# Kernel optimization log

Hardware: AMD Instinct MI355X
Metric: run time of the kernel (lower is better)

The kernel has to match this reference:

```python
import jax, jax.numpy as jnp
import numpy as np

UNITS = 1024
B, T, D1, D2 = 16, 2048, 1024, 1024


def setup_inputs() -> dict:
    key = jax.random.key(0)
    ks = jax.random.split(key, 9)
    s1 = 1.0 / np.sqrt(D1)
    s2 = 1.0 / np.sqrt(D2)
    sw = 1.0 / np.sqrt(2 * UNITS)
    return {
        "sequences1": jax.random.normal(ks[0], (B, T, D1), dtype=jnp.float32),
        "sequences2": jax.random.normal(ks[1], (B, T, D2), dtype=jnp.float32),
        "W1_kernel": jax.random.normal(ks[2], (D1, UNITS), dtype=jnp.float32) * s1,
        "W1_bias": jnp.zeros((UNITS,), dtype=jnp.float32),
        "W2_kernel": jax.random.normal(ks[3], (D2, UNITS), dtype=jnp.float32) * s2,
        "W2_bias": jnp.zeros((UNITS,), dtype=jnp.float32),
        "W_kernel": jax.random.normal(ks[4], (2 * UNITS, UNITS), dtype=jnp.float32) * sw,
        "W_bias": jnp.zeros((UNITS,), dtype=jnp.float32),
        "context_vector": jax.random.uniform(ks[5], (UNITS, 1), dtype=jnp.float32),
    }


def reference(sequences1, sequences2, W1_kernel, W1_bias, W2_kernel, W2_bias,
              W_kernel, W_bias, context_vector):
    # Dense projections: [B,T,D] @ [D,U] -> [B,T,U]
    features1 = jnp.einsum("btd,du->btu", sequences1, W1_kernel) + W1_bias
    features2 = jnp.einsum("btd,du->btu", sequences2, W2_kernel) + W2_bias
    fusion = jnp.concatenate([features1, features2], axis=-1)  # [B,T,2U]
    features = jnp.tanh(jnp.einsum("btk,ku->btu", fusion, W_kernel) + W_bias)  # [B,T,U]
    # scores: [B,T,U] @ [U,1] -> [B,T,1]; softmax over time (axis=1)
    scores = jnp.einsum("btu,uo->bto", features, context_vector)
    attn = jax.nn.softmax(scores, axis=1)  # [B,T,1]
    # weighted sum over time: [B,T] x [B,T,U] -> [B,U]
    seq_rep = jnp.einsum("bt,btu->bu", attn[..., 0], features)
    return seq_rep
```

## Files before the change

kernel.cpp:

```cpp
#include <hip/hip_runtime.h>
#include <hip/hip_bf16.h>
#include <cstdint>
#include <cstddef>


typedef __attribute__((ext_vector_type(8))) short short8;
typedef __attribute__((ext_vector_type(4))) float f32x4;
typedef __attribute__((ext_vector_type(4))) unsigned short u16x4;

#define DEVINL static __device__ __forceinline__

DEVINL unsigned short bf16_rne(float f) {
  uint32_t u = __float_as_uint(f);
  uint32_t r = (u + 0x7FFFu + ((u >> 16) & 1u)) >> 16;
  return (unsigned short)r;
}
DEVINL float bf16f(unsigned short h) { return __uint_as_float(((uint32_t)h) << 16); }

DEVINL int lds_chunk(int r, int q) { return (r << 2) + (q ^ ((r >> 1) & 3)); }

DEVINL void gload_lds16(const void* g, void* l) {
  __builtin_amdgcn_global_load_lds(
      (const __attribute__((address_space(1))) uint32_t*)g,
      (__attribute__((address_space(3))) uint32_t*)l, 16, 0, 0);
}

DEVINL float fast_tanh(float x) {
  float e = __expf(2.0f * x);
  return 1.0f - 2.0f / (e + 1.0f);
}

template<int MFR, int NFR, int WMW, int WNW, int MODE>
__global__ __launch_bounds__(WMW*WNW*64, 2)
void gemm3x(const float* __restrict__ A1, const float* __restrict__ A2,
            const unsigned short* __restrict__ Bh, const unsigned short* __restrict__ Bl,
            unsigned short* __restrict__ Mh, unsigned short* __restrict__ Ml,
            const float* __restrict__ bias_eff, const float* __restrict__ cvec,
            void* __restrict__ feat, float* __restrict__ scores)
{
  constexpr int WTM = MFR * 16, WTN = NFR * 16;
  constexpr int BM = WMW * WTM, BN = WNW * WTN;
  constexpr int NT = WMW * WNW * 64;
  constexpr int NWAVES = NT / 64;
  constexpr int AHI = 0, ALO = BM * 32, BHI = 2 * BM * 32, BLO = 2 * BM * 32 + BN * 32;
  constexpr int BUFSZ = 2 * BM * 32 + 2 * BN * 32;
  constexpr int AITER = (BM * 4) / NT;
  constexpr int KSTEPS = (MODE == 0) ? 32 : 64;
  static_assert((BM * 4) % NT == 0, "A staging mapping");
  static_assert((BN * 4) % (64 * NWAVES) == 0, "B staging mapping");

  __shared__ __attribute__((aligned(16))) unsigned short sm[2 * BUFSZ];

  const int tid = threadIdx.x;
  const int lane = tid & 63;
  const int wid = tid >> 6;
  const int wm = wid / WNW, wn = wid % WNW;

  int bm, bn, zsel, bkoff;
  if constexpr (MODE == 0) {
    bm = blockIdx.x; bn = blockIdx.y; zsel = blockIdx.z; bkoff = zsel * 1024;
  } else {
    int g = blockIdx.x;
    int xcd = g & 7, idx = g >> 3;
    bn = idx & 7;
    bm = (xcd << 5) | (idx >> 3);
    zsel = 0; bkoff = 0;
  }
  const float* Asel = (MODE == 0) ? (zsel ? A2 : A1) : nullptr;

  f32x4 acc[MFR][NFR];
  #pragma unroll
  for (int i = 0; i < MFR; ++i)
    #pragma unroll
    for (int j = 0; j < NFR; ++j) acc[i][j] = (f32x4){0.f, 0.f, 0.f, 0.f};

  float areg[AITER][8];

  auto stageB = [&](int bsel, int k0) {
    #pragma unroll
    for (int c = 0; c < (BN * 4) / 64 / NWAVES; ++c) {
      int call = wid + c * NWAVES;
      int chunk = call * 64 + lane;
      int r = chunk >> 2, qs = chunk & 3;
      int ql = qs ^ ((r >> 1) & 3);
      size_t gidx = (size_t)(bn * BN + r) * 2048 + (size_t)(bkoff + k0 + ql * 8);
      gload_lds16(Bh + gidx, (void*)&sm[bsel * BUFSZ + BHI + call * 512]);
      gload_lds16(Bl + gidx, (void*)&sm[bsel * BUFSZ + BLO + call * 512]);
    }
  };

  auto stageA_load = [&](int k0) {
    #pragma unroll
    for (int it = 0; it < AITER; ++it) {
      int e = tid + it * NT;
      int r = e >> 2, q = e & 3;
      size_t row = (size_t)(bm * BM + r);
      const float* src;
      if constexpr (MODE == 0) {
        src = Asel + row * 1024 + (k0 + q * 8);
      } else {
        const float* base = (k0 < 1024) ? A1 : A2;
        src = base + row * 1024 + ((k0 & 1023) + q * 8);
      }
      float4 v0 = *(const float4*)(src);
      float4 v1 = *(const float4*)(src + 4);
      areg[it][0] = v0.x; areg[it][1] = v0.y; areg[it][2] = v0.z; areg[it][3] = v0.w;
      areg[it][4] = v1.x; areg[it][5] = v1.y; areg[it][6] = v1.z; areg[it][7] = v1.w;
    }
  };

  auto stageA_write = [&](int bsel) {
    #pragma unroll
    for (int it = 0; it < AITER; ++it) {
      int e = tid + it * NT;
      int r = e >> 2, q = e & 3;
      short8 hi, lo;
      #pragma unroll
      for (int j = 0; j < 8; ++j) {
        float x = areg[it][j];
        unsigned short h = bf16_rne(x);
        hi[j] = (short)h;
        lo[j] = (short)bf16_rne(x - bf16f(h));
      }
      int ch = lds_chunk(r, q);
      *(short8*)(&sm[bsel * BUFSZ + AHI + ch * 8]) = hi;
      *(short8*)(&sm[bsel * BUFSZ + ALO + ch * 8]) = lo;
    }
  };

  auto compute = [&](int bsel) {
    short8 bh[NFR], bl[NFR];
    #pragma unroll
    for (int nf = 0; nf < NFR; ++nf) {
      int nl = wn * WTN + nf * 16 + (lane & 15);
      int ch = lds_chunk(nl, lane >> 4);
      bh[nf] = *(const short8*)(&sm[bsel * BUFSZ + BHI + ch * 8]);
      bl[nf] = *(const short8*)(&sm[bsel * BUFSZ + BLO + ch * 8]);
    }
    #pragma unroll
    for (int mf = 0; mf < MFR; ++mf) {
      int ml = wm * WTM + mf * 16 + (lane & 15);
      int ch = lds_chunk(ml, lane >> 4);
      short8 ah = *(const short8*)(&sm[bsel * BUFSZ + AHI + ch * 8]);
      short8 al = *(const short8*)(&sm[bsel * BUFSZ + ALO + ch * 8]);
      #pragma unroll
      for (int nf = 0; nf < NFR; ++nf) {
        acc[mf][nf] = __builtin_amdgcn_mfma_f32_16x16x32_bf16(ah, bh[nf], acc[mf][nf], 0, 0, 0);
        acc[mf][nf] = __builtin_amdgcn_mfma_f32_16x16x32_bf16(al, bh[nf], acc[mf][nf], 0, 0, 0);
        acc[mf][nf] = __builtin_amdgcn_mfma_f32_16x16x32_bf16(ah, bl[nf], acc[mf][nf], 0, 0, 0);
      }
    }
  };

  stageB(0, 0);
  stageA_load(0);
  stageA_write(0);
  __syncthreads();

  for (int t = 0; t < KSTEPS; ++t) {
    int cur = t & 1;
    if (t + 1 < KSTEPS) { stageB(cur ^ 1, (t + 1) * 32); stageA_load((t + 1) * 32); }
    compute(cur);
    if (t + 1 < KSTEPS) stageA_write(cur ^ 1);
    __syncthreads();
  }

  if constexpr (MODE == 0) {
    const int zoff = zsel * 1024;
    #pragma unroll
    for (int nf = 0; nf < NFR; ++nf) {
      int u = bn * BN + wn * WTN + nf * 16 + (lane & 15);
      #pragma unroll
      for (int mf = 0; mf < MFR; ++mf) {
        int d0 = bm * BM + wm * WTM + mf * 16 + ((lane >> 4) << 2);
        u16x4 h4, l4;
        #pragma unroll
        for (int i = 0; i < 4; ++i) {
          float v = acc[mf][nf][i];
          unsigned short h = bf16_rne(v);
          h4[i] = h;
          l4[i] = bf16_rne(v - bf16f(h));
        }
        *(u16x4*)(Mh + (size_t)u * 2048 + zoff + d0) = h4;
        *(u16x4*)(Ml + (size_t)u * 2048 + zoff + d0) = l4;
      }
    }
  } else {
    float bia[NFR], cvv[NFR];
    int ncol[NFR];
    #pragma unroll
    for (int nf = 0; nf < NFR; ++nf) {
      ncol[nf] = bn * BN + wn * WTN + nf * 16 + (lane & 15);
      bia[nf] = bias_eff[ncol[nf]];
      cvv[nf] = cvec[ncol[nf]];
    }
    #pragma unroll
    for (int mf = 0; mf < MFR; ++mf) {
      int r0 = bm * BM + wm * WTM + mf * 16 + ((lane >> 4) << 2);
      float sp[4] = {0.f, 0.f, 0.f, 0.f};
      #pragma unroll
      for (int nf = 0; nf < NFR; ++nf) {
        #pragma unroll
        for (int i = 0; i < 4; ++i) {
          float f = fast_tanh(acc[mf][nf][i] + bia[nf]);
          size_t idx = (size_t)(r0 + i) * 1024 + ncol[nf];
          if constexpr (MODE == 1) ((float*)feat)[idx] = f;
          else                     ((unsigned short*)feat)[idx] = bf16_rne(f);
          sp[i] += f * cvv[nf];
        }
      }
      #pragma unroll
      for (int i = 0; i < 4; ++i) {
        float s = sp[i];
        s += __shfl_xor(s, 1); s += __shfl_xor(s, 2);
        s += __shfl_xor(s, 4); s += __shfl_xor(s, 8);
        if ((lane & 15) == 0) atomicAdd(&scores[r0 + i], s);
      }
    }
  }
}

__global__ __launch_bounds__(256)
void split_transpose_w(const float* __restrict__ W,
                       unsigned short* __restrict__ Wt_h,
                       unsigned short* __restrict__ Wt_l)
{
  __shared__ float tsm[64][68];
  const int j0 = blockIdx.x * 64, u0 = blockIdx.y * 64;
  const int tid = threadIdx.x;
  const int jr = tid >> 4, uc = (tid & 15) * 4;
  #pragma unroll
  for (int rr = 0; rr < 4; ++rr) {
    int j = jr + rr * 16;
    float4 v = *(const float4*)(W + (size_t)(j0 + j) * 1024 + u0 + uc);
    tsm[j][uc + 0] = v.x; tsm[j][uc + 1] = v.y;
    tsm[j][uc + 2] = v.z; tsm[j][uc + 3] = v.w;
  }
  __syncthreads();
  const int ul = tid & 63, seg = tid >> 6;
  short8 h8[2], l8[2];
  #pragma unroll
  for (int k = 0; k < 16; ++k) {
    float v = tsm[seg * 16 + k][ul];
    unsigned short h = bf16_rne(v);
    h8[k >> 3][k & 7] = (short)h;
    l8[k >> 3][k & 7] = (short)bf16_rne(v - bf16f(h));
  }
  size_t ob = (size_t)(u0 + ul) * 2048 + j0 + seg * 16;
  *(short8*)(Wt_h + ob) = h8[0];
  *(short8*)(Wt_h + ob + 8) = h8[1];
  *(short8*)(Wt_l + ob) = l8[0];
  *(short8*)(Wt_l + ob + 8) = l8[1];
}

__global__ __launch_bounds__(256)
void bias_eff_k(const float* __restrict__ b1, const float* __restrict__ b2,
                const float* __restrict__ W, const float* __restrict__ Wb,
                float* __restrict__ bias_eff)
{
  int u = blockIdx.x * 256 + threadIdx.x;
  float acc = Wb[u];
  for (int j = 0; j < 1024; ++j) {
    acc = fmaf(b1[j], W[(size_t)j * 1024 + u], acc);
    acc = fmaf(b2[j], W[(size_t)(j + 1024) * 1024 + u], acc);
  }
  bias_eff[u] = acc;
}

__global__ __launch_bounds__(256)
void softmax_t(const float* __restrict__ scores, float* __restrict__ weights)
{
  __shared__ float rmax[4], rsum[4];
  const int b = blockIdx.x, tid = threadIdx.x;
  const int lane = tid & 63, wid = tid >> 6;
  float v[8];
  float mx = -3.0e38f;
  #pragma unroll
  for (int i = 0; i < 8; ++i) {
    v[i] = scores[b * 2048 + i * 256 + tid];
    mx = fmaxf(mx, v[i]);
  }
  #pragma unroll
  for (int m = 1; m < 64; m <<= 1) mx = fmaxf(mx, __shfl_xor(mx, m));
  if (lane == 0) rmax[wid] = mx;
  __syncthreads();
  mx = fmaxf(fmaxf(rmax[0], rmax[1]), fmaxf(rmax[2], rmax[3]));
  float s = 0.f;
  #pragma unroll
  for (int i = 0; i < 8; ++i) { v[i] = __expf(v[i] - mx); s += v[i]; }
  #pragma unroll
  for (int m = 1; m < 64; m <<= 1) s += __shfl_xor(s, m);
  if (lane == 0) rsum[wid] = s;
  __syncthreads();
  s = rsum[0] + rsum[1] + rsum[2] + rsum[3];
  float inv = 1.0f / s;
  #pragma unroll
  for (int i = 0; i < 8; ++i) weights[b * 2048 + i * 256 + tid] = v[i] * inv;
}

template<int F32>
__global__ __launch_bounds__(256)
void weighted_sum_k(const float* __restrict__ weights, const void* __restrict__ feat,
                    float* __restrict__ out)
{
  const int b = blockIdx.x >> 4, tc = blockIdx.x & 15;
  const int tid = threadIdx.x;
  float a0 = 0.f, a1 = 0.f, a2 = 0.f, a3 = 0.f;
  const int t0 = tc * 128;
  for (int t = 0; t < 128; ++t) {
    int row = b * 2048 + t0 + t;
    float wgt = weights[row];
    if constexpr (F32) {
      float4 f = *((const float4*)feat + (size_t)row * 256 + tid);
      a0 = fmaf(wgt, f.x, a0); a1 = fmaf(wgt, f.y, a1);
      a2 = fmaf(wgt, f.z, a2); a3 = fmaf(wgt, f.w, a3);
    } else {
      u16x4 f = *((const u16x4*)feat + (size_t)row * 256 + tid);
      a0 = fmaf(wgt, bf16f(f[0]), a0); a1 = fmaf(wgt, bf16f(f[1]), a1);
      a2 = fmaf(wgt, bf16f(f[2]), a2); a3 = fmaf(wgt, bf16f(f[3]), a3);
    }
  }
  float* o = out + b * 1024 + tid * 4;
  atomicAdd(o + 0, a0); atomicAdd(o + 1, a1);
  atomicAdd(o + 2, a2); atomicAdd(o + 3, a3);
}

extern "C" void kernel_launch(void* const* d_in, const int* in_sizes, int n_in,
                              void* d_out, int out_size, void* d_ws, size_t ws_size,
                              hipStream_t stream)
{
  (void)in_sizes; (void)n_in;
  const float* S1 = (const float*)d_in[0];
  const float* S2 = (const float*)d_in[1];
  const float* W1 = (const float*)d_in[2];
  const float* b1 = (const float*)d_in[3];
  const float* W2 = (const float*)d_in[4];
  const float* b2 = (const float*)d_in[5];
  const float* Wk = (const float*)d_in[6];
  const float* Wb = (const float*)d_in[7];
  const float* cv = (const float*)d_in[8];

  char* p = (char*)d_ws;
  unsigned short* Mt_h = (unsigned short*)p; p += (size_t)1024 * 2048 * 2;
  unsigned short* Mt_l = (unsigned short*)p; p += (size_t)1024 * 2048 * 2;
  unsigned short* Wt_h = (unsigned short*)p; p += (size_t)1024 * 2048 * 2;
  unsigned short* Wt_l = (unsigned short*)p; p += (size_t)1024 * 2048 * 2;
  float* bias_eff = (float*)p; p += 4096;
  float* scores   = (float*)p; p += (size_t)32768 * 4;
  float* weights  = (float*)p; p += (size_t)32768 * 4;
  void* feat = (void*)p;
  size_t base = (size_t)(p - (char*)d_ws);
  bool f32feat = (ws_size >= base + (size_t)32768 * 1024 * 4);

  hipMemsetAsync(scores, 0, 32768 * 4, stream);
  hipMemsetAsync(d_out, 0, (size_t)out_size * 4, stream);

  split_transpose_w<<<dim3(32, 16, 1), 256, 0, stream>>>(Wk, Wt_h, Wt_l);
  bias_eff_k<<<dim3(4, 1, 1), 256, 0, stream>>>(b1, b2, Wk, Wb, bias_eff);

  gemm3x<4, 2, 2, 2, 0><<<dim3(8, 16, 2), 256, 0, stream>>>(
      W1, W2, Wt_h, Wt_l, Mt_h, Mt_l, nullptr, nullptr, nullptr, nullptr);

  if (f32feat)
    gemm3x<4, 4, 2, 2, 1><<<dim3(2048, 1, 1), 256, 0, stream>>>(
        S1, S2, Mt_h, Mt_l, nullptr, nullptr, bias_eff, cv, feat, scores);
  else
    gemm3x<4, 4, 2, 2, 2><<<dim3(2048, 1, 1), 256, 0, stream>>>(
        S1, S2, Mt_h, Mt_l, nullptr, nullptr, bias_eff, cv, feat, scores);

  softmax_t<<<dim3(16, 1, 1), 256, 0, stream>>>(scores, weights);

  if (f32feat)
    weighted_sum_k<1><<<dim3(256, 1, 1), 256, 0, stream>>>(weights, feat, (float*)d_out);
  else
    weighted_sum_k<0><<<dim3(256, 1, 1), 256, 0, stream>>>(weights, feat, (float*)d_out);
}
```

Baseline: 818.4 us.

## Pre-split activations to bf16 hi/lo and use 32x32 MFMA main GEMM

When the workspace is large enough, a new pass first splits the fp32 input sequences into bf16 hi and lo planes. A new main GEMM kernel then streams those planes straight into LDS and runs 32x32x16 bf16 MFMAs with the three-product split, fused with the bias, tanh and score epilogue. The aim is to take the fp32-to-bf16 conversion out of the GEMM inner loop and use larger MFMA tiles, at the cost of an extra full read and write of the activations (about 256MB). The bias precompute is parallelised over K with atomics, and the weighted sum uses twice as many blocks.

```diff
diff --git a/kernel.cpp b/kernel.cpp
--- a/kernel.cpp
+++ b/kernel.cpp
@@ -6,6 +6,7 @@
 
 typedef __attribute__((ext_vector_type(8))) short short8;
 typedef __attribute__((ext_vector_type(4))) float f32x4;
+typedef __attribute__((ext_vector_type(16))) float f32x16;
 typedef __attribute__((ext_vector_type(4))) unsigned short u16x4;
 
 #define DEVINL static __device__ __forceinline__
@@ -28,6 +29,136 @@
 DEVINL float fast_tanh(float x) {
   float e = __expf(2.0f * x);
   return 1.0f - 2.0f / (e + 1.0f);
+}
+
+__global__ __launch_bounds__(256)
+void split_x(const float* __restrict__ S1, const float* __restrict__ S2,
+             unsigned short* __restrict__ Xh, unsigned short* __restrict__ Xl)
+{
+  const int stride = gridDim.x * blockDim.x;
+  for (int c = blockIdx.x * blockDim.x + threadIdx.x; c < 32768 * 256; c += stride) {
+    int row = c >> 8, col = (c & 255) << 3;
+    const float* src = (col < 1024) ? (S1 + (size_t)row * 1024 + col)
+                                    : (S2 + (size_t)row * 1024 + (col - 1024));
+    float4 v0 = *(const float4*)src;
+    float4 v1 = *(const float4*)(src + 4);
+    float xs[8] = {v0.x, v0.y, v0.z, v0.w, v1.x, v1.y, v1.z, v1.w};
+    short8 h, l;
+    #pragma unroll
+    for (int j = 0; j < 8; ++j) {
+      unsigned short hh = bf16_rne(xs[j]);
+      h[j] = (short)hh;
+      l[j] = (short)bf16_rne(xs[j] - bf16f(hh));
+    }
+    size_t o = (size_t)row * 2048 + col;
+    *(short8*)(Xh + o) = h;
+    *(short8*)(Xl + o) = l;
+  }
+}
+
+template<int F32>
+__global__ __launch_bounds__(256, 3)
+void main32(const unsigned short* __restrict__ Xh, const unsigned short* __restrict__ Xl,
+            const unsigned short* __restrict__ Bh, const unsigned short* __restrict__ Bl,
+            const float* __restrict__ bias_eff, const float* __restrict__ cvec,
+            void* __restrict__ feat, float* __restrict__ scores)
+{
+  constexpr int TSZ = 128 * 16;
+  constexpr int BUFSZ = 4 * TSZ;
+  __shared__ __attribute__((aligned(16))) unsigned short sm[2 * BUFSZ];
+
+  const int tid = threadIdx.x, lane = tid & 63, wid = tid >> 6;
+  const int wm = wid >> 1, wn = wid & 1;
+
+  const int g = blockIdx.x;
+  const int idx = g >> 3;
+  const int bn = idx & 7;
+  const int bm = ((g & 7) << 5) | (idx >> 3);
+
+  f32x16 acc[2][2];
+  #pragma unroll
+  for (int mf = 0; mf < 2; ++mf)
+    #pragma unroll
+    for (int nf = 0; nf < 2; ++nf)
+      #pragma unroll
+      for (int i = 0; i < 16; ++i) acc[mf][nf][i] = 0.f;
+
+  auto stage = [&](int bsel, int k0) {
+    int r = tid >> 1;
+    int q = (tid & 1) ^ ((r >> 2) & 1);
+    size_t ga = (size_t)(bm * 128 + r) * 2048 + (size_t)(k0 + q * 8);
+    size_t gb = (size_t)(bn * 128 + r) * 2048 + (size_t)(k0 + q * 8);
+    unsigned short* dst = &sm[bsel * BUFSZ + wid * 512];
+    gload_lds16(Xh + ga, dst);
+    gload_lds16(Xl + ga, dst + TSZ);
+    gload_lds16(Bh + gb, dst + 2 * TSZ);
+    gload_lds16(Bl + gb, dst + 3 * TSZ);
+  };
+
+  auto ldfrag = [&](int bsel, int t, int band) -> short8 {
+    int r = band + (lane & 31);
+    int q = (lane >> 5) ^ ((r >> 2) & 1);
+    return *(const short8*)(&sm[bsel * BUFSZ + t * TSZ + (r * 2 + q) * 8]);
+  };
+
+  auto compute = [&](int bsel) {
+    short8 bh[2], bl[2];
+    #pragma unroll
+    for (int nf = 0; nf < 2; ++nf) {
+      bh[nf] = ldfrag(bsel, 2, wn * 64 + nf * 32);
+      bl[nf] = ldfrag(bsel, 3, wn * 64 + nf * 32);
+    }
+    #pragma unroll
+    for (int mf = 0; mf < 2; ++mf) {
+      short8 ah = ldfrag(bsel, 0, wm * 64 + mf * 32);
+      short8 al = ldfrag(bsel, 1, wm * 64 + mf * 32);
+      #pragma unroll
+      for (int nf = 0; nf < 2; ++nf) {
+        acc[mf][nf] = __builtin_amdgcn_mfma_f32_32x32x16_bf16(ah, bh[nf], acc[mf][nf], 0, 0, 0);
+        acc[mf][nf] = __builtin_amdgcn_mfma_f32_32x32x16_bf16(al, bh[nf], acc[mf][nf], 0, 0, 0);
+        acc[mf][nf] = __builtin_amdgcn_mfma_f32_32x32x16_bf16(ah, bl[nf], acc[mf][nf], 0, 0, 0);
+      }
+    }
+  };
+
+  stage(0, 0);
+  __syncthreads();
+  for (int t = 0; t < 128; ++t) {
+    int cur = t & 1;
+    if (t + 1 < 128) stage(cur ^ 1, (t + 1) * 16);
+    compute(cur);
+    __syncthreads();
+  }
+
+  const int cl = lane & 31, hi6 = lane >> 5;
+  float bia[2], cvv[2];
+  int ncol[2];
+  #pragma unroll
+  for (int nf = 0; nf < 2; ++nf) {
+    ncol[nf] = bn * 128 + wn * 64 + nf * 32 + cl;
+    bia[nf] = bias_eff[ncol[nf]];
+    cvv[nf] = cvec[ncol[nf]];
+  }
+  #pragma unroll
+  for (int mf = 0; mf < 2; ++mf) {
+    int rbase = bm * 128 + wm * 64 + mf * 32 + 4 * hi6;
+    #pragma unroll
+    for (int reg = 0; reg < 16; ++reg) {
+      int row = rbase + (reg & 3) + 8 * (reg >> 2);
+      float s = 0.f;
+      #pragma unroll
+      for (int nf = 0; nf < 2; ++nf) {
+        float f = fast_tanh(acc[mf][nf][reg] + bia[nf]);
+        size_t idx = (size_t)row * 1024 + ncol[nf];
+        if (F32) ((float*)feat)[idx] = f;
+        else     ((unsigned short*)feat)[idx] = bf16_rne(f);
+        s += f * cvv[nf];
+      }
+      s += __shfl_xor(s, 1); s += __shfl_xor(s, 2); s += __shfl_xor(s, 4);
+      s += __shfl_xor(s, 8); s += __shfl_xor(s, 16);
+      if (cl == 0) atomicAdd(&scores[row], s);
+    }
+  }
 }
 
 template<int MFR, int NFR, int WMW, int WNW, int MODE>
@@ -254,17 +385,17 @@
 }
 
 __global__ __launch_bounds__(256)
-void bias_eff_k(const float* __restrict__ b1, const float* __restrict__ b2,
-                const float* __restrict__ W, const float* __restrict__ Wb,
-                float* __restrict__ bias_eff)
+void bias_eff2(const float* __restrict__ b1, const float* __restrict__ b2,
+               const float* __restrict__ W, float* __restrict__ bias_eff)
 {
   int u = blockIdx.x * 256 + threadIdx.x;
-  float acc = Wb[u];
-  for (int j = 0; j < 1024; ++j) {
+  int j0 = blockIdx.y * 128;
+  float acc = 0.f;
+  for (int j = j0; j < j0 + 128; ++j) {
     acc = fmaf(b1[j], W[(size_t)j * 1024 + u], acc);
     acc = fmaf(b2[j], W[(size_t)(j + 1024) * 1024 + u], acc);
   }
-  bias_eff[u] = acc;
+  atomicAdd(&bias_eff[u], acc);
 }
 
 __global__ __launch_bounds__(256)
@@ -303,11 +434,11 @@
 void weighted_sum_k(const float* __restrict__ weights, const void* __restrict__ feat,
                     float* __restrict__ out)
 {
-  const int b = blockIdx.x >> 4, tc = blockIdx.x & 15;
+  const int b = blockIdx.x >> 5, tc = blockIdx.x & 31;
   const int tid = threadIdx.x;
   float a0 = 0.f, a1 = 0.f, a2 = 0.f, a3 = 0.f;
-  const int t0 = tc * 128;
-  for (int t = 0; t < 128; ++t) {
+  const int t0 = tc * 64;
+  for (int t = 0; t < 64; ++t) {
     int row = b * 2048 + t0 + t;
     float wgt = weights[row];
     if constexpr (F32) {
@@ -345,33 +476,46 @@
   unsigned short* Mt_l = (unsigned short*)p; p += (size_t)1024 * 2048 * 2;
   unsigned short* Wt_h = (unsigned short*)p; p += (size_t)1024 * 2048 * 2;
   unsigned short* Wt_l = (unsigned short*)p; p += (size_t)1024 * 2048 * 2;
-  float* bias_eff = (float*)p; p += 4096;
+  float* bias_eff = (float*)p; p += 16384;
   float* scores   = (float*)p; p += (size_t)32768 * 4;
   float* weights  = (float*)p; p += (size_t)32768 * 4;
-  void* feat = (void*)p;
   size_t base = (size_t)(p - (char*)d_ws);
-  bool f32feat = (ws_size >= base + (size_t)32768 * 1024 * 4);
+
+  const size_t szX   = (size_t)32768 * 2048 * 2;
+  const size_t szF32 = (size_t)32768 * 1024 * 4;
+  bool tierA   = ws_size >= base + 2 * szX + szF32;
+  bool f32feat = ws_size >= base + szF32;
 
   hipMemsetAsync(scores, 0, 32768 * 4, stream);
   hipMemsetAsync(d_out, 0, (size_t)out_size * 4, stream);
+  hipMemcpyAsync(bias_eff, Wb, 1024 * 4, hipMemcpyDeviceToDevice, stream);
 
   split_transpose_w<<<dim3(32, 16, 1), 256, 0, stream>>>(Wk, Wt_h, Wt_l);
-  bias_eff_k<<<dim3(4, 1, 1), 256, 0, stream>>>(b1, b2, Wk, Wb, bias_eff);
+  bias_eff2<<<dim3(4, 8, 1), 256, 0, stream>>>(b1, b2, Wk, bias_eff);
 
   gemm3x<4, 2, 2, 2, 0><<<dim3(8, 16, 2), 256, 0, stream>>>(
       W1, W2, Wt_h, Wt_l, Mt_h, Mt_l, nullptr, nullptr, nullptr, nullptr);
 
-  if (f32feat)
+  if (tierA) {
+    unsigned short* Xh = (unsigned short*)(p);
+    unsigned short* Xl = (unsigned short*)(p + szX);
+    void* feat = (void*)(p + 2 * szX);
+    split_x<<<dim3(2048, 1, 1), 256, 0, stream>>>(S1, S2, Xh, Xl);
+    main32<1><<<dim3(2048, 1, 1), 256, 0, stream>>>(
+        Xh, Xl, Mt_h, Mt_l, bias_eff, cv, feat, scores);
+    softmax_t<<<dim3(16, 1, 1), 256, 0, stream>>>(scores, weights);
+    weighted_sum_k<1><<<dim3(512, 1, 1), 256, 0, stream>>>(weights, feat, (float*)d_out);
+  } else if (f32feat) {
+    void* feat = (void*)p;
     gemm3x<4, 4, 2, 2, 1><<<dim3(2048, 1, 1), 256, 0, stream>>>(
         S1, S2, Mt_h, Mt_l, nullptr, nullptr, bias_eff, cv, feat, scores);
-  else
+    softmax_t<<<dim3(16, 1, 1), 256, 0, stream>>>(scores, weights);
+    weighted_sum_k<1><<<dim3(512, 1, 1), 256, 0, stream>>>(weights, feat, (float*)d_out);
+  } else {
+    void* feat = (void*)p;
     gemm3x<4, 4, 2, 2, 2><<<dim3(2048, 1, 1), 256, 0, stream>>>(
         S1, S2, Mt_h, Mt_l, nullptr, nullptr, bias_eff, cv, feat, scores);
-
-  softmax_t<<<dim3(16, 1, 1), 256, 0, stream>>>(scores, weights);
-
-  if (f32feat)
-    weighted_sum_k<1><<<dim3(256, 1, 1), 256, 0, stream>>>(weights, feat, (float*)d_out);
-  else
-    weighted_sum_k<0><<<dim3(256, 1, 1), 256, 0, stream>>>(weights, feat, (float*)d_out);
-}
+    softmax_t<<<dim3(16, 1, 1), 256, 0, stream>>>(scores, weights);
+    weighted_sum_k<0><<<dim3(512, 1, 1), 256, 0, stream>>>(weights, feat, (float*)d_out);
+  }
+}
```

After: 981.8 us. 1.2x slower.
